# Kernel optimization log

Hardware: AMD Instinct MI355X
Metric: run time of the kernel (lower is better)

The kernel has to match this reference:

```python
import jax, jax.numpy as jnp
import numpy as np

B, N, ND, ED = 4, 24, 13, 12          # batch, num_nodes, node feat dim, edge feat dim
H, NH, HD = 256, 8, 32                # hidden, heads, head dim (H == NH*HD)
L, T = 64, 1000                       # transformer layers, max_timestep
_SCALE = 1.0 / float(np.sqrt(H))      # torch divides by sqrt(node_dim)=sqrt(256)


def _ln(x, g, b):
    m = x.mean(-1, keepdims=True)
    v = ((x - m) ** 2).mean(-1, keepdims=True)
    return (x - m) / jnp.sqrt(v + 1e-5) * g + b


def setup_inputs() -> dict:
    key = jax.random.key(0)
    it = iter(jax.random.split(key, 40))
    def w(*s):
        return (jax.random.normal(next(it), s) * 0.02).astype(jnp.float32)
    z = lambda *s: jnp.zeros(s, jnp.float32)
    o = lambda *s: jnp.ones(s, jnp.float32)
    d = {}
    d['nodes'] = jax.random.normal(next(it), (B, N, ND), jnp.float32)
    d['edges'] = jax.random.normal(next(it), (B, N, N, ED), jnp.float32)
    d['conds'] = jax.random.randint(next(it), (B,), 0, T)
    # input MLPs
    d['inN_w1'] = w(ND, H); d['inN_b1'] = z(H); d['inN_w2'] = w(H, H); d['inN_b2'] = z(H)
    d['inE_w1'] = w(ED, H); d['inE_b1'] = z(H); d['inE_w2'] = w(H, H); d['inE_b2'] = z(H)
    d['inC_w1'] = w(T, H);  d['inC_b1'] = z(H); d['inC_w2'] = w(H, H); d['inC_b2'] = z(H)
    # stacked per-layer params (leading dim L, scanned)
    d['qkv_w'] = w(L, H, 3 * H); d['qkv_b'] = z(L, 3 * H)
    d['no_w'] = w(L, H, H); d['no_b'] = z(L, H)
    d['eo_w'] = w(L, H, H); d['eo_b'] = z(L, H)
    d['ln1n_g'] = o(L, H); d['ln1n_b'] = z(L, H)
    d['ln1e_g'] = o(L, H); d['ln1e_b'] = z(L, H)
    d['mn_w1'] = w(L, H, 4 * H); d['mn_b1'] = z(L, 4 * H)
    d['mn_w2'] = w(L, 4 * H, H); d['mn_b2'] = z(L, H)
    d['me_w1'] = w(L, H, 4 * H); d['me_b1'] = z(L, 4 * H)
    d['me_w2'] = w(L, 4 * H, H); d['me_b2'] = z(L, H)
    d['ln2n_g'] = o(L, H); d['ln2n_b'] = z(L, H)
    d['ln2e_g'] = o(L, H); d['ln2e_b'] = z(L, H)
    # output MLPs
    d['outN_w1'] = w(H, H); d['outN_b1'] = z(H); d['outN_w2'] = w(H, ND); d['outN_b2'] = z(ND)
    d['outE_w1'] = w(H, H); d['outE_b1'] = z(H); d['outE_w2'] = w(H, ED); d['outE_b2'] = z(ED)
    return d


def _forward(nodes, edges, conds,
             inN_w1, inN_b1, inN_w2, inN_b2, inE_w1, inE_b1, inE_w2, inE_b2,
             inC_w1, inC_b1, inC_w2, inC_b2,
             qkv_w, qkv_b, no_w, no_b, eo_w, eo_b,
             ln1n_g, ln1n_b, ln1e_g, ln1e_b,
             mn_w1, mn_b1, mn_w2, mn_b2, me_w1, me_b1, me_w2, me_b2,
             ln2n_g, ln2n_b, ln2e_g, ln2e_b,
             outN_w1, outN_b1, outN_w2, outN_b2, outE_w1, outE_b1, outE_w2, outE_b2):
    relu = jax.nn.relu
    c = jax.nn.one_hot(conds, T, dtype=nodes.dtype)
    c = relu(relu(c @ inC_w1 + inC_b1) @ inC_w2 + inC_b2)          # (B,H)
    n = relu(relu(nodes @ inN_w1 + inN_b1) @ inN_w2 + inN_b2)      # (B,N,H)
    e = relu(relu(edges @ inE_w1 + inE_b1) @ inE_w2 + inE_b2)      # (B,N,N,H)

    def layer(carry, p):
        n, e = carry
        (qw, qb, nw, nb, ew, eb, g1n, b1n, g1e, b1e,
         w1n, bb1n, w2n, bb2n, w1e, bb1e, w2e, bb2e, g2n, b2n, g2e, b2e) = p
        nc = n + c[:, None, :]
        q, k, v = jnp.split(nc @ qw + qb, 3, axis=-1)
        q = q.reshape(B, N, NH, HD); k = k.reshape(B, N, NH, HD); v = v.reshape(B, N, NH, HD)
        s5 = jnp.einsum('bihd,bjhd->bijhd', q, k) * _SCALE          # (B,N,N,NH,HD)
        ne5 = s5 + e.reshape(B, N, N, NH, HD)                       # edge-biased scores
        attn = jax.nn.softmax(ne5.sum(-1), axis=2)                  # (B,N,N,NH)
        wv = jnp.einsum('bijh,bjhd->bihd', attn, v).reshape(B, N, H)
        an = _ln(wv @ nw + nb + n, g1n, b1n)
        ae = _ln(relu(ne5.reshape(B, N, N, H) @ ew + eb) + e, g1e, b1e)
        n2 = _ln(relu(an @ w1n + bb1n) @ w2n + bb2n + an, g2n, b2n)
        e2 = _ln(relu(ae @ w1e + bb1e) @ w2e + bb2e + ae, g2e, b2e)
        return (n2, e2), None

    stacked = (qkv_w, qkv_b, no_w, no_b, eo_w, eo_b, ln1n_g, ln1n_b, ln1e_g, ln1e_b,
               mn_w1, mn_b1, mn_w2, mn_b2, me_w1, me_b1, me_w2, me_b2,
               ln2n_g, ln2n_b, ln2e_g, ln2e_b)
    (n, e), _ = jax.lax.scan(layer, (n, e), stacked)
    out_n = relu(n @ outN_w1 + outN_b1) @ outN_w2 + outN_b2
    out_e = relu(e @ outE_w1 + outE_b1) @ outE_w2 + outE_b2
    return out_n, out_e


def reference(nodes, edges, conds,
              inN_w1, inN_b1, inN_w2, inN_b2, inE_w1, inE_b1, inE_w2, inE_b2,
              inC_w1, inC_b1, inC_w2, inC_b2,
              qkv_w, qkv_b, no_w, no_b, eo_w, eo_b,
              ln1n_g, ln1n_b, ln1e_g, ln1e_b,
              mn_w1, mn_b1, mn_w2, mn_b2, me_w1, me_b1, me_w2, me_b2,
              ln2n_g, ln2n_b, ln2e_g, ln2e_b,
              outN_w1, outN_b1, outN_w2, outN_b2, outE_w1, outE_b1, outE_w2, outE_b2):
    return _forward(nodes, edges, conds,
                    inN_w1, inN_b1, inN_w2, inN_b2, inE_w1, inE_b1, inE_w2, inE_b2,
                    inC_w1, inC_b1, inC_w2, inC_b2,
                    qkv_w, qkv_b, no_w, no_b, eo_w, eo_b,
                    ln1n_g, ln1n_b, ln1e_g, ln1e_b,
                    mn_w1, mn_b1, mn_w2, mn_b2, me_w1, me_b1, me_w2, me_b2,
                    ln2n_g, ln2n_b, ln2e_g, ln2e_b,
                    outN_w1, outN_b1, outN_w2, outN_b2, outE_w1, outE_b1, outE_w2, outE_b2)
```

## Files before the change

kernel.cpp:

```cpp
#include <hip/hip_runtime.h>

typedef _Float16 half_t;
typedef _Float16 f16x8 __attribute__((ext_vector_type(8)));
typedef _Float16 f16x4 __attribute__((ext_vector_type(4)));
typedef float f32x4 __attribute__((ext_vector_type(4)));

#define BB 4
#define NNODE 24
#define NLAYER 64
#define SCALE_QK 0.0625f

#define WS_C     0
#define WS_N     1024
#define WS_QKV   25600
#define WS_E     99328
#define WS_WV    689152
#define WS_NACC  713728
#define WS_AE32  738304
#define WS_AE16  1328128
#define WS_AN16  1623040
#define WS_EPART 1635328
#define EPART_SLICE 589824
#define WS_WTF   3994624
#define SLOT_F16 1376256
#define OFF_QKVT 0
#define OFF_NOT  196608
#define OFF_EOT  262144
#define OFF_MN1T 327680
#define OFF_MN2T 589824
#define OFF_ME1T 851968
#define OFF_ME2T 1114112
#define OFF_INE2T  (3*SLOT_F16)
#define OFF_OUTE1T (3*SLOT_F16 + 65536)

struct Params {
  const float *nodes, *edges; const int* conds;
  const float *inN_w1,*inN_b1,*inN_w2,*inN_b2;
  const float *inE_w1,*inE_b1,*inE_w2,*inE_b2;
  const float *inC_w1,*inC_b1,*inC_w2,*inC_b2;
  const float *qkv_w,*qkv_b,*no_w,*no_b,*eo_w,*eo_b;
  const float *ln1n_g,*ln1n_b,*ln1e_g,*ln1e_b;
  const float *mn_w1,*mn_b1,*mn_w2,*mn_b2,*me_w1,*me_b1,*me_w2,*me_b2;
  const float *ln2n_g,*ln2n_b,*ln2e_g,*ln2e_b;
  const float *outN_w1,*outN_b1,*outN_w2,*outN_b2,*outE_w1,*outE_b1,*outE_w2,*outE_b2;
  float* ws; float* out;
};

template<int NT, int KS, int MT, int LDAH>
__device__ __forceinline__ void gemm_rs_acc(const half_t* __restrict__ WT, int ldb,
                                            const char* __restrict__ A,
                                            f32x4 (&acc)[NT][MT]) {
  const int lane = threadIdx.x & 63;
  const int wv = threadIdx.x >> 6;
  const int l15 = lane & 15;
  const int kg = lane >> 4;
  f16x8 b[NT][KS];
#pragma unroll
  for (int nt = 0; nt < NT; ++nt) {
    const int col = (nt * 8 + wv) * 16 + l15;
#pragma unroll
    for (int ks = 0; ks < KS; ++ks)
      b[nt][ks] = *(const f16x8*)(WT + (size_t)col * ldb + ks * 32 + kg * 8);
  }
#pragma unroll
  for (int m = 0; m < MT; ++m) {
    f16x8 a[KS];
    const int row = m * 16 + l15;
#pragma unroll
    for (int ks = 0; ks < KS; ++ks)
      a[ks] = *(const f16x8*)(A + row * (LDAH * 2) + (((ks * 32 + kg * 8) * 2) ^ ((row & 7) << 4)));
#pragma unroll
    for (int ks = 0; ks < KS; ++ks)
#pragma unroll
      for (int nt = 0; nt < NT; ++nt)
        acc[nt][m] = __builtin_amdgcn_mfma_f32_16x16x32_f16(a[ks], b[nt][ks], acc[nt][m], 0, 0, 0);
  }
}

template<int NT, int KS, int MT, int LDAH, typename EPI>
__device__ __forceinline__ void gemm_rs(const half_t* __restrict__ WT, int ldb,
                                        const char* __restrict__ A, EPI epi) {
  f32x4 acc[NT][MT];
#pragma unroll
  for (int nt = 0; nt < NT; ++nt)
#pragma unroll
    for (int m = 0; m < MT; ++m) {
      f32x4 z = {0.f, 0.f, 0.f, 0.f};
      acc[nt][m] = z;
    }
  gemm_rs_acc<NT, KS, MT, LDAH>(WT, ldb, A, acc);
#pragma unroll
  for (int nt = 0; nt < NT; ++nt)
#pragma unroll
    for (int m = 0; m < MT; ++m)
      epi(nt, m, acc[nt][m]);
}

template<int NTW, int KT, int MT, int LDA, int LDB, typename EPI>
__device__ __forceinline__ void run_gemm_s(const half_t* __restrict__ WT,
                                           const char* __restrict__ A,
                                           EPI epi) {
  const int lane = threadIdx.x & 63;
  const int wv = threadIdx.x >> 6;
  const int l15 = lane & 15;
  const int kg = lane >> 4;
  constexpr int NC = KT / 8;
// ... 19 lines not shown
    f16x8 a[8][MT];
#pragma unroll
    for (int q = 0; q < 8; ++q) {
      const int k0 = (kc * 8 + q) * 32 + kg * 8;
#pragma unroll
      for (int m = 0; m < MT; ++m) {
        const int row = m * 16 + l15;
        a[q][m] = *(const f16x8*)(A + row * (LDA * 2) + ((k0 * 2) ^ ((row & 7) << 4)));
      }
    }
#pragma unroll
    for (int n = 0; n < NTW; ++n) {
      const int c = kc * NTW + n;
      if (c + 1 < TC) ldb(c + 1, (c + 1) & 1);
#pragma unroll
      for (int q = 0; q < 8; ++q)
#pragma unroll
        for (int m = 0; m < MT; ++m)
          acc[n][m] = __builtin_amdgcn_mfma_f32_16x16x32_f16(a[q][m], bb[c & 1][q], acc[n][m], 0, 0, 0);
    }
  }
#pragma unroll
  for (int n = 0; n < NTW; ++n) epi(n, acc[n]);
}

__device__ void conv_matrix_tile(const float* __restrict__ src, half_t* __restrict__ dst,
                                 int K, int Nn, int tk, int tn, char* smem) {
  float* tl = (float*)smem;
  const int t = threadIdx.x;
  const int c = t & 63;
  const int r0 = t >> 6;
  for (int r = r0; r < 64; r += 8)
    tl[r * 65 + c] = src[(size_t)(tk * 64 + r) * Nn + tn * 64 + c];
  __syncthreads();
  for (int r = r0; r < 64; r += 8)
    dst[(size_t)(tn * 64 + r) * K + tk * 64 + c] = (half_t)tl[c * 65 + r];
  __syncthreads();
}

__device__ void conv_layer_tile(const Params& p, half_t* slot, int lw, int tile, char* smem) {
  if (tile < 48)       { conv_matrix_tile(p.qkv_w + (size_t)lw*196608, slot+OFF_QKVT, 256, 768, tile & 3, tile >> 2, smem); }
  else if (tile < 64)  { int t2 = tile-48;  conv_matrix_tile(p.no_w  + (size_t)lw*65536,  slot+OFF_NOT,  256, 256, t2 & 3,  t2 >> 2, smem); }
  else if (tile < 80)  { int t2 = tile-64;  conv_matrix_tile(p.eo_w  + (size_t)lw*65536,  slot+OFF_EOT,  256, 256, t2 & 3,  t2 >> 2, smem); }
  else if (tile < 144) { int t2 = tile-80;  conv_matrix_tile(p.mn_w1 + (size_t)lw*262144, slot+OFF_MN1T, 256, 1024, t2 & 3, t2 >> 2, smem); }
  else if (tile < 208) { int t2 = tile-144; conv_matrix_tile(p.mn_w2 + (size_t)lw*262144, slot+OFF_MN2T, 1024, 256, t2 & 15, t2 >> 4, smem); }
  else if (tile < 272) { int t2 = tile-208; conv_matrix_tile(p.me_w1 + (size_t)lw*262144, slot+OFF_ME1T, 256, 1024, t2 & 3, t2 >> 2, smem); }
  else                 { int t2 = tile-272; conv_matrix_tile(p.me_w2 + (size_t)lw*262144, slot+OFF_ME2T, 1024, 256, t2 & 15, t2 >> 4, smem); }
}

__global__ __launch_bounds__(512, 2) void k_embedA(Params p) {
  __shared__ __align__(16) char smem[17024];
  const int bid = blockIdx.x, tid = threadIdx.x;
  float* ws = p.ws;
  half_t* wt = (half_t*)(ws + WS_WTF);
  if (bid < 4) {
    const int b = bid;
    const int cond = p.conds[b];
    float* t1 = (float*)smem;
    if (tid < 256) t1[tid] = fmaxf(p.inC_w1[(size_t)cond * 256 + tid] + p.inC_b1[tid], 0.f);
    __syncthreads();
    if (tid < 256) {
      float s = p.inC_b2[tid];
      for (int k = 0; k < 256; ++k) s += t1[k] * p.inC_w2[(size_t)k * 256 + tid];
      ws[WS_C + b * 256 + tid] = fmaxf(s, 0.f);
    }
  } else {
    for (int job = bid - 4; job < 704; job += 128) {
      if (job < 336)      conv_layer_tile(p, wt, 0, job, smem);
      else if (job < 672) conv_layer_tile(p, wt + SLOT_F16, 1, job - 336, smem);
      else if (job < 688) { int t2 = job - 672; conv_matrix_tile(p.inE_w2,  wt + OFF_INE2T,  256, 256, t2 & 3, t2 >> 2, smem); }
      else                { int t2 = job - 688; conv_matrix_tile(p.outE_w1, wt + OFF_OUTE1T, 256, 256, t2 & 3, t2 >> 2, smem); }
    }
  }
}

__global__ __launch_bounds__(512, 2) void k_embedB(Params p) {
  __shared__ __align__(16) char smem[24640];
  const int bid = blockIdx.x, tid = threadIdx.x;
  const int lane = tid & 63, wv = tid >> 6, l15 = lane & 15, kg = lane >> 4;
  float* ws = p.ws;
  half_t* wt = (half_t*)(ws + WS_WTF);
  float* e0 = ws + WS_E;
  float* n0 = ws + WS_N;
  float* qkv0 = ws + WS_QKV;
  if (bid < 96) {
    const int b = bid / NNODE, i = bid % NNODE;
    float* eb = (float*)smem;
    char* t16 = smem + 2048;
    for (int idx = tid; idx < 24 * 12; idx += 512)
      eb[idx] = p.edges[((size_t)(b * NNODE + i) * NNODE + idx / 12) * 12 + idx % 12];
    __syncthreads();
    for (int idx = tid; idx < 32 * 32; idx += 512) {
      int r = idx >> 5, kb = idx & 31, k0 = kb * 8;
      f16x8 v;
#pragma unroll
      for (int j = 0; j < 8; ++j) v[j] = (half_t)0.f;
      if (r < NNODE) {
#pragma unroll
        for (int j = 0; j < 8; ++j) {
          int col = k0 + j;
          float s = p.inE_b1[col];
          for (int kk = 0; kk < 12; ++kk) s += eb[r * 12 + kk] * p.inE_w1[kk * 256 + col];
          v[j] = (half_t)fmaxf(s, 0.f);
        }
      }
      *(f16x8*)(t16 + r * 512 + ((k0 * 2) ^ ((r & 7) << 4))) = v;
    }
    __syncthreads();
    run_gemm_s<2, 8, 2, 256, 256>(wt + OFF_INE2T, t16,
      [&](int n, f32x4 (&accn)[2]) {
        const int col = (n * 8 + wv) * 16 + l15;
        const float bcol = p.inE_b2[col];
#pragma unroll
        for (int m = 0; m < 2; ++m)
#pragma unroll
          for (int r4 = 0; r4 < 4; ++r4) {
            const int row = m * 16 + kg * 4 + r4;
            if (row < NNODE)
              e0[((size_t)(b * NNODE + i) * NNODE + row) * 256 + col] = fmaxf(accn[m][r4] + bcol, 0.f);
          }
      });
  } else {
    const int nb = bid - 96, b = nb >> 1, hf = nb & 1, i0 = hf * 12;
    float* nd = (float*)smem;
    float* t1 = (float*)(smem + 1024);
    char* nc16 = smem + 16384;
    for (int idx = tid; idx < 12 * 13; idx += 512)
      nd[(idx / 13) * 16 + (idx % 13)] = p.nodes[(size_t)(b * NNODE + i0 + idx / 13) * 13 + idx % 13];
    __syncthreads();
    for (int idx = tid; idx < 12 * 256; idx += 512) {
      int r = idx >> 8, col = idx & 255;
      float s = p.inN_b1[col];
      for (int kk = 0; kk < 13; ++kk) s += nd[r * 16 + kk] * p.inN_w1[kk * 256 + col];
      t1[r * 257 + col] = fmaxf(s, 0.f);
    }
    __syncthreads();
    {
      int col = tid & 255, rh = tid >> 8;
      float a6[6] = {0.f, 0.f, 0.f, 0.f, 0.f, 0.f};
      for (int k = 0; k < 256; ++k) {
        float w = p.inN_w2[(size_t)k * 256 + col];
#pragma unroll
        for (int r = 0; r < 6; ++r) a6[r] += t1[(rh * 6 + r) * 257 + k] * w;
      }
      const float* cb = ws + WS_C + b * 256;
#pragma unroll
      for (int r = 0; r < 6; ++r) {
        int row = rh * 6 + r;
        float y = fmaxf(a6[r] + p.inN_b2[col], 0.f);
        n0[(size_t)(b * NNODE + i0 + row) * 256 + col] = y;
        *(half_t*)(nc16 + row * 512 + ((col * 2) ^ ((row & 7) << 4))) = (half_t)(y + cb[col]);
      }
      if (rh == 0)
        for (int row = 12; row < 16; ++row)
          *(half_t*)(nc16 + row * 512 + ((col * 2) ^ ((row & 7) << 4))) = (half_t)0.f;
    }
    __syncthreads();
    run_gemm_s<6, 8, 1, 256, 256>(wt + OFF_QKVT, nc16,
      [&](int n, f32x4 (&accn)[1]) {
        const int col = (n * 8 + wv) * 16 + l15;
#pragma unroll
        for (int r4 = 0; r4 < 4; ++r4) {
          const int row = kg * 4 + r4;
          if (row < 12)
            qkv0[(size_t)(b * NNODE + i0 + row) * 768 + col] = accn[0][r4] + p.qkv_b[col];
        }
      });
  }
}

__global__ __launch_bounds__(512, 2) void k_attn(Params p, int lyr) {
  __shared__ __align__(16) char smem[94464];
  const int bid = blockIdx.x, tid = threadIdx.x;
  const int lane = tid & 63, wv = tid >> 6, l15 = lane & 15, kg = lane >> 4;
  float* ws = p.ws;
  half_t* wt = (half_t*)(ws + WS_WTF);
  const float* qkv_in = ws + WS_QKV;
  const half_t* slot = wt + (size_t)(lyr % 3) * SLOT_F16;

  if (bid >= 96) {
    if (lyr + 2 < NLAYER) {
      half_t* dslot = wt + (size_t)((lyr + 2) % 3) * SLOT_F16;
      for (int tile = bid - 96; tile < 336; tile += 126)
        conv_layer_tile(p, dslot, lyr + 2, tile, smem);
    }
    return;
  }
  const int b = bid / NNODE, i = bid % NNODE;
  const size_t rowbase = (size_t)(b * NNODE + i) * NNODE;
  char* ne5 = smem;
  float* e32 = (float*)(smem + 16384);
  float* v32 = (float*)(smem + 41344);
  float* psum = (float*)(smem + 65920);
  float* sc = (float*)(smem + 68992);
  float* aef = (float*)(smem + 69760);
  float* ae32 = ws + WS_AE32;
  half_t* ae16g = (half_t*)(ws + WS_AE16);
  const half_t* epart = (const half_t*)(ws + WS_EPART);

  for (int idx = tid; idx < 32 * 32; idx += 512) {
    int r = idx >> 5, kb = idx & 31, k0 = kb * 8;
    f16x8 v;
#pragma unroll
    for (int j = 0; j < 8; ++j) v[j] = (half_t)0.f;
    if (r < NNODE) {
      const size_t row = rowbase + r;
      float x[8];
      if (lyr == 0) {
        const f32x4 a = *(const f32x4*)(ws + WS_E + row * 256 + k0);
        const f32x4 b4 = *(const f32x4*)(ws + WS_E + row * 256 + k0 + 4);
#pragma unroll
        for (int j = 0; j < 4; ++j) { x[j] = a[j]; x[4 + j] = b4[j]; }
      } else {
        const float* mb2 = p.me_b2 + (size_t)(lyr - 1) * 256;
        const f32x4 a = *(const f32x4*)(ae32 + row * 256 + k0);
        const f32x4 b4 = *(const f32x4*)(ae32 + row * 256 + k0 + 4);
#pragma unroll
        for (int j = 0; j < 4; ++j) { x[j] = a[j] + mb2[k0 + j]; x[4 + j] = b4[j] + mb2[k0 + 4 + j]; }
#pragma unroll
        for (int hb = 0; hb < 8; ++hb) {
          f16x8 pv = *(const f16x8*)(epart + (size_t)hb * EPART_SLICE + row * 256 + k0);
#pragma unroll
          for (int j = 0; j < 8; ++j) x[j] += (float)pv[j];
        }
        float s = 0.f, s2 = 0.f;
#pragma unroll
        for (int j = 0; j < 8; ++j) { s += x[j]; s2 += x[j] * x[j]; }
#pragma unroll
        for (int off = 16; off; off >>= 1) { s += __shfl_xor(s, off); s2 += __shfl_xor(s2, off); }
        float mean = s * (1.f / 256.f);
        float rstd = rsqrtf(s2 * (1.f / 256.f) - mean * mean + 1e-5f);
        const float* g = p.ln2e_g + (size_t)(lyr - 1) * 256;
        const float* bv = p.ln2e_b + (size_t)(lyr - 1) * 256;
#pragma unroll
        for (int j = 0; j < 8; ++j) x[j] = (x[j] - mean) * rstd * g[k0 + j] + bv[k0 + j];
      }
      const float* qp = qkv_in + (size_t)(b * NNODE + i) * 768 + k0;
      const float* kp = qkv_in + (size_t)(b * NNODE + r) * 768 + 256 + k0;
      f32x4 q0 = *(const f32x4*)qp, q1 = *(const f32x4*)(qp + 4);
      f32x4 k0v = *(const f32x4*)kp, k1v = *(const f32x4*)(kp + 4);
      float ps = 0.f;
#pragma unroll
      for (int j = 0; j < 4; ++j) {
        float f0 = SCALE_QK * q0[j] * k0v[j] + x[j];
        float f1 = SCALE_QK * q1[j] * k1v[j] + x[4 + j];
        v[j] = (half_t)f0; v[4 + j] = (half_t)f1;
        ps += f0 + f1;
      }
#pragma unroll
      for (int j = 0; j < 4; ++j) { e32[r * 260 + k0 + j] = x[j]; e32[r * 260 + k0 + 4 + j] = x[4 + j]; }
      psum[r * 32 + kb] = ps;
    }
    *(f16x8*)(ne5 + r * 512 + ((k0 * 2) ^ ((r & 7) << 4))) = v;
  }
  __syncthreads();
  for (int idx = tid; idx < 24 * 256; idx += 512) {
    int j = idx >> 8, d = idx & 255;
    v32[j * 256 + d] = qkv_in[(size_t)(b * NNODE + j) * 768 + 512 + d];
  }
  if (tid < 192) {
    int hq = tid & 7;
    sc[tid] = psum[(tid >> 3) * 32 + hq * 4] + psum[(tid >> 3) * 32 + hq * 4 + 1] +
              psum[(tid >> 3) * 32 + hq * 4 + 2] + psum[(tid >> 3) * 32 + hq * 4 + 3];
  }
  __syncthreads();
  if (tid < 8) {
    const int h = tid;
    float mx = -1e30f;
#pragma unroll
    for (int j = 0; j < 24; ++j) mx = fmaxf(mx, sc[j * 8 + h]);
    float ex[24]; float ssum = 0.f;
#pragma unroll
    for (int j = 0; j < 24; ++j) { ex[j] = __expf(sc[j * 8 + h] - mx); ssum += ex[j]; }
    float inv = 1.f / ssum;
#pragma unroll
    for (int j = 0; j < 24; ++j) sc[j * 8 + h] = ex[j] * inv;
  }
  __syncthreads();
  if (tid < 256) {
    const int d = tid, h = d >> 5;
    float a = 0.f;
#pragma unroll
    for (int j = 0; j < 24; ++j) a += sc[j * 8 + h] * v32[j * 256 + d];
    ws[WS_WV + (size_t)(b * NNODE + i) * 256 + d] = a;
  }
  {
    const float* eob = p.eo_b + (size_t)lyr * 256;
    gemm_rs<2, 8, 2, 256>(slot + OFF_EOT, 256, ne5,
      [&](int nt, int m, f32x4 v) {
        const int col = (nt * 8 + wv) * 16 + l15;
#pragma unroll
        for (int r4 = 0; r4 < 4; ++r4) {
          const int row = m * 16 + kg * 4 + r4;
          if (row < NNODE)
            aef[row * 257 + col] = fmaxf(v[r4] + eob[col], 0.f) + e32[row * 260 + col];
        }
      });
  }
  __syncthreads();
  {
    const float* g = p.ln1e_g + (size_t)lyr * 256;
    const float* bv = p.ln1e_b + (size_t)lyr * 256;
    for (int r = wv; r < NNODE; r += 8) {
      float x[4];
#pragma unroll
      for (int j = 0; j < 4; ++j) x[j] = aef[r * 257 + lane * 4 + j];
      float s = x[0] + x[1] + x[2] + x[3];
      float s2 = x[0]*x[0] + x[1]*x[1] + x[2]*x[2] + x[3]*x[3];
#pragma unroll
      for (int off = 32; off; off >>= 1) { s += __shfl_xor(s, off); s2 += __shfl_xor(s2, off); }
      float mean = s * (1.f / 256.f);
      float rstd = rsqrtf(s2 * (1.f / 256.f) - mean * mean + 1e-5f);
      f16x4 hv; f32x4 yv;
#pragma unroll
      for (int j = 0; j < 4; ++j) {
        int c = lane * 4 + j;
        float y = (x[j] - mean) * rstd * g[c] + bv[c];
        yv[j] = y; hv[j] = (half_t)y;
      }
      *(f32x4*)(ae32 + (rowbase + r) * 256 + lane * 4) = yv;
      *(f16x4*)(ae16g + (rowbase + r) * 256 + lane * 4) = hv;
    }
  }
}

__global__ __launch_bounds__(512, 2) void k_mlp1(Params p, int lyr) {
  __shared__ __align__(16) char smem[73728];
  const int bid = blockIdx.x, tid = threadIdx.x;
  const int lane = tid & 63, wv = tid >> 6, l15 = lane & 15, kg = lane >> 4;
  float* ws = p.ws;
  half_t* wt = (half_t*)(ws + WS_WTF);
  const half_t* slot = wt + (size_t)(lyr % 3) * SLOT_F16;

  if (bid < 192) {
    const int rb = bid >> 3, hb = bid & 7;
    const int row0 = rb * 96;
    char* A16 = smem;
    char* hl = smem + 49152;
    const half_t* aeg = (const half_t*)(ws + WS_AE16) + (size_t)row0 * 256;
    for (int idx = tid; idx < 96 * 32; idx += 512) {
      int r = idx >> 5, c8 = idx & 31;
      f16x8 v = *(const f16x8*)(aeg + r * 256 + c8 * 8);
      *(f16x8*)(A16 + r * 512 + ((c8 * 16) ^ ((r & 7) << 4))) = v;
    }
    __syncthreads();
    const float* mb1 = p.me_b1 + (size_t)lyr * 1024 + hb * 128;
    gemm_rs<1, 8, 6, 256>(slot + OFF_ME1T + (size_t)(hb * 128) * 256, 256, A16,
      [&](int nt, int m, f32x4 v) {
        const int colb = wv * 16 + l15;
        const float bc = mb1[colb];
#pragma unroll
        for (int r4 = 0; r4 < 4; ++r4) {
          const int row = m * 16 + kg * 4 + r4;
          *(half_t*)(hl + row * 256 + ((colb * 2) ^ ((row & 7) << 4))) = (half_t)fmaxf(v[r4] + bc, 0.f);
        }
      });
    __syncthreads();
    half_t* ep = (half_t*)(ws + WS_EPART) + (size_t)hb * EPART_SLICE + (size_t)row0 * 256;
    gemm_rs<2, 4, 6, 128>(slot + OFF_ME2T + hb * 128, 1024, hl,
      [&](int nt, int m, f32x4 v) {
        const int col = (nt * 8 + wv) * 16 + l15;
#pragma unroll
        for (int r4 = 0; r4 < 4; ++r4)
          ep[(size_t)(m * 16 + kg * 4 + r4) * 256 + col] = (half_t)v[r4];
      });
  } else {
    const int nb = bid - 192, r0 = nb * 12;
    char* A16 = smem;
    float* nin = (float*)(smem + 8192);
    float* anf = (float*)(smem + 20528);
    float* n_acc = ws + WS_NACC;
    {
      for (int r = wv; r < 12; r += 8) {
        const int row = r0 + r;
        const int c = lane * 4;
        if (lyr == 0) {
          f32x4 v = *(const f32x4*)(ws + WS_N + (size_t)row * 256 + c);
          *(f32x4*)(nin + r * 257 + c) = v;
        } else {
          f32x4 x = *(const f32x4*)(n_acc + (size_t)row * 256 + c);
          float s = x[0] + x[1] + x[2] + x[3];
          float s2 = x[0]*x[0] + x[1]*x[1] + x[2]*x[2] + x[3]*x[3];
#pragma unroll
          for (int off = 32; off; off >>= 1) { s += __shfl_xor(s, off); s2 += __shfl_xor(s2, off); }
          float mean = s * (1.f / 256.f);
          float rstd = rsqrtf(s2 * (1.f / 256.f) - mean * mean + 1e-5f);
          const float* g = p.ln2n_g + (size_t)(lyr - 1) * 256;
          const float* bv = p.ln2n_b + (size_t)(lyr - 1) * 256;
          f32x4 y;
#pragma unroll
          for (int j = 0; j < 4; ++j) y[j] = (x[j] - mean) * rstd * g[c + j] + bv[c + j];
          *(f32x4*)(nin + r * 257 + c) = y;
        }
      }
    }
    for (int idx = tid; idx < 16 * 32; idx += 512) {
      int r = idx >> 5, c8 = idx & 31;
      f16x8 v;
      if (r < 12) {
        const float* sp = ws + WS_WV + (size_t)(r0 + r) * 256 + c8 * 8;
        f32x4 a = *(const f32x4*)sp, b4 = *(const f32x4*)(sp + 4);
#pragma unroll
        for (int j = 0; j < 4; ++j) { v[j] = (half_t)a[j]; v[4 + j] = (half_t)b4[j]; }
      } else {
#pragma unroll
        for (int j = 0; j < 8; ++j) v[j] = (half_t)0.f;
      }
      *(f16x8*)(A16 + r * 512 + ((c8 * 16) ^ ((r & 7) << 4))) = v;
    }
    __syncthreads();
    {
      const float* nob = p.no_b + (size_t)lyr * 256;
      gemm_rs<2, 8, 1, 256>(slot + OFF_NOT, 256, A16,
        [&](int nt, int m, f32x4 v) {
          const int col = (nt * 8 + wv) * 16 + l15;
#pragma unroll
          for (int r4 = 0; r4 < 4; ++r4) {
            const int row = kg * 4 + r4;
            if (row < 12)
              anf[row * 257 + col] = v[r4] + nob[col] + nin[row * 257 + col];
          }
        });
    }
    __syncthreads();
    {
      const float* g = p.ln1n_g + (size_t)lyr * 256;
      const float* bv = p.ln1n_b + (size_t)lyr * 256;
      const float* mb2 = p.mn_b2 + (size_t)lyr * 256;
      half_t* an16g = (half_t*)(ws + WS_AN16);
      for (int r = wv; r < 12; r += 8) {
        float x[4];
#pragma unroll
        for (int j = 0; j < 4; ++j) x[j] = anf[r * 257 + lane * 4 + j];
        float s = x[0] + x[1] + x[2] + x[3];
        float s2 = x[0]*x[0] + x[1]*x[1] + x[2]*x[2] + x[3]*x[3];
#pragma unroll
        for (int off = 32; off; off >>= 1) { s += __shfl_xor(s, off); s2 += __shfl_xor(s2, off); }
        float mean = s * (1.f / 256.f);
        float rstd = rsqrtf(s2 * (1.f / 256.f) - mean * mean + 1e-5f);
        f16x4 hv; f32x4 av;
#pragma unroll
        for (int j = 0; j < 4; ++j) {
          int c = lane * 4 + j;
          float y = (x[j] - mean) * rstd * g[c] + bv[c];
          hv[j] = (half_t)y;
          av[j] = y + mb2[c];
        }
        *(f16x4*)(an16g + (size_t)(r0 + r) * 256 + lane * 4) = hv;
        *(f32x4*)(ws + WS_NACC + (size_t)(r0 + r) * 256 + lane * 4) = av;
      }
    }
  }
}

__global__ __launch_bounds__(512, 2) void k_mn(Params p, int lyr) {
  __shared__ __align__(16) char smem[73728];
  const int hb = blockIdx.x, tid = threadIdx.x;
  const int lane = tid & 63, wv = tid >> 6, l15 = lane & 15, kg = lane >> 4;
  float* ws = p.ws;
  half_t* wt = (half_t*)(ws + WS_WTF);
  const half_t* slot = wt + (size_t)(lyr % 3) * SLOT_F16;
  char* A16 = smem;
  char* hl = smem + 49152;
  const half_t* ang = (const half_t*)(ws + WS_AN16);
  for (int idx = tid; idx < 96 * 32; idx += 512) {
    int r = idx >> 5, c8 = idx & 31;
    f16x8 v = *(const f16x8*)(ang + (size_t)r * 256 + c8 * 8);
    *(f16x8*)(A16 + r * 512 + ((c8 * 16) ^ ((r & 7) << 4))) = v;
  }
  __syncthreads();
  const float* mb1 = p.mn_b1 + (size_t)lyr * 1024 + hb * 128;
  gemm_rs<1, 8, 6, 256>(slot + OFF_MN1T + (size_t)(hb * 128) * 256, 256, A16,
    [&](int nt, int m, f32x4 v) {
      const int colb = wv * 16 + l15;
      const float bc = mb1[colb];
#pragma unroll
      for (int r4 = 0; r4 < 4; ++r4) {
        const int row = m * 16 + kg * 4 + r4;
        *(half_t*)(hl + row * 256 + ((colb * 2) ^ ((row & 7) << 4))) = (half_t)fmaxf(v[r4] + bc, 0.f);
      }
    });
  __syncthreads();
  float* n_acc = ws + WS_NACC;
  gemm_rs<2, 4, 6, 128>(slot + OFF_MN2T + hb * 128, 1024, hl,
    [&](int nt, int m, f32x4 v) {
      const int col = (nt * 8 + wv) * 16 + l15;
#pragma unroll
      for (int r4 = 0; r4 < 4; ++r4)
        atomicAdd(&n_acc[(size_t)(m * 16 + kg * 4 + r4) * 256 + col], v[r4]);
    });
}

__global__ __launch_bounds__(512, 2) void k_qkv(Params p, int lyr) {
  __shared__ __align__(16) char smem[49152];
  const int bid = blockIdx.x, tid = threadIdx.x;
  const int lane = tid & 63, wv = tid >> 6, l15 = lane & 15, kg = lane >> 4;
  float* ws = p.ws;
  half_t* wt = (half_t*)(ws + WS_WTF);
  char* nc16 = smem;
  const float* n_acc = ws + WS_NACC;
  const float* g = p.ln2n_g + (size_t)lyr * 256;
  const float* bv = p.ln2n_b + (size_t)lyr * 256;
  for (int r = wv; r < 96; r += 8) {
    const int c = lane * 4;
    const float* cb = ws + WS_C + (r / NNODE) * 256;
    f32x4 x = *(const f32x4*)(n_acc + (size_t)r * 256 + c);
    float s = x[0] + x[1] + x[2] + x[3];
    float s2 = x[0]*x[0] + x[1]*x[1] + x[2]*x[2] + x[3]*x[3];
#pragma unroll
    for (int off = 32; off; off >>= 1) { s += __shfl_xor(s, off); s2 += __shfl_xor(s2, off); }
    float mean = s * (1.f / 256.f);
    float rstd = rsqrtf(s2 * (1.f / 256.f) - mean * mean + 1e-5f);
    f16x4 hv;
#pragma unroll
    for (int j = 0; j < 4; ++j)
      hv[j] = (half_t)((x[j] - mean) * rstd * g[c + j] + bv[c + j] + cb[c + j]);
    *(f16x4*)(nc16 + r * 512 + ((c * 2) ^ ((r & 7) << 4))) = hv;
  }
  __syncthreads();
  const int col0 = bid * 128;
  const half_t* slotN = wt + (size_t)((lyr + 1) % 3) * SLOT_F16;
  const float* qb = p.qkv_b + (size_t)(lyr + 1) * 768;
  float* qkv_out = ws + WS_QKV;
  gemm_rs<1, 8, 6, 256>(slotN + OFF_QKVT + (size_t)col0 * 256, 256, nc16,
    [&](int nt, int m, f32x4 v) {
      const int col = col0 + wv * 16 + l15;
#pragma unroll
      for (int r4 = 0; r4 < 4; ++r4) {
        const int row = m * 16 + kg * 4 + r4;
        qkv_out[(size_t)row * 768 + col] = v[r4] + qb[col];
      }
    });
}

__global__ __launch_bounds__(512, 2) void k_out(Params p) {
  __shared__ __align__(16) char smem[49472];
  const int bid = blockIdx.x, tid = threadIdx.x;
  const int lane = tid & 63, wv = tid >> 6, l15 = lane & 15, kg = lane >> 4;
  float* ws = p.ws;
  half_t* wt = (half_t*)(ws + WS_WTF);
  const float* ae32 = ws + WS_AE32;
  const half_t* epart = (const half_t*)(ws + WS_EPART);
  if (bid < 96) {
    const int b = bid / NNODE, i = bid % NNODE;
    const size_t rowbase = (size_t)(b * NNODE + i) * NNODE;
    char* A16 = smem;
    float* h2f = (float*)(smem + 16384);
    const float* mb2 = p.me_b2 + (size_t)63 * 256;
    const float* g = p.ln2e_g + (size_t)63 * 256;
    const float* bvv = p.ln2e_b + (size_t)63 * 256;
    for (int idx = tid; idx < 32 * 32; idx += 512) {
      int r = idx >> 5, kb = idx & 31, k0 = kb * 8;
      f16x8 v;
#pragma unroll
      for (int j = 0; j < 8; ++j) v[j] = (half_t)0.f;
      if (r < NNODE) {
        const size_t row = rowbase + r;
        float x[8];
        const f32x4 a = *(const f32x4*)(ae32 + row * 256 + k0);
        const f32x4 b4 = *(const f32x4*)(ae32 + row * 256 + k0 + 4);
#pragma unroll
        for (int j = 0; j < 4; ++j) { x[j] = a[j] + mb2[k0 + j]; x[4 + j] = b4[j] + mb2[k0 + 4 + j]; }
#pragma unroll
        for (int hb = 0; hb < 8; ++hb) {
          f16x8 pv = *(const f16x8*)(epart + (size_t)hb * EPART_SLICE + row * 256 + k0);
#pragma unroll
          for (int j = 0; j < 8; ++j) x[j] += (float)pv[j];
        }
        float s = 0.f, s2 = 0.f;
#pragma unroll
        for (int j = 0; j < 8; ++j) { s += x[j]; s2 += x[j] * x[j]; }
#pragma unroll
        for (int off = 16; off; off >>= 1) { s += __shfl_xor(s, off); s2 += __shfl_xor(s2, off); }
        float mean = s * (1.f / 256.f);
        float rstd = rsqrtf(s2 * (1.f / 256.f) - mean * mean + 1e-5f);
#pragma unroll
        for (int j = 0; j < 8; ++j)
          v[j] = (half_t)((x[j] - mean) * rstd * g[k0 + j] + bvv[k0 + j]);
      }
      *(f16x8*)(A16 + r * 512 + ((k0 * 2) ^ ((r & 7) << 4))) = v;
    }
    __syncthreads();
    run_gemm_s<2, 8, 2, 256, 256>(wt + OFF_OUTE1T, A16,
      [&](int n, f32x4 (&accn)[2]) {
        const int col = (n * 8 + wv) * 16 + l15;
#pragma unroll
        for (int m = 0; m < 2; ++m)
#pragma unroll
          for (int r4 = 0; r4 < 4; ++r4) {
            const int row = m * 16 + kg * 4 + r4;
            h2f[row * 257 + col] = (row < NNODE) ? fmaxf(accn[m][r4] + p.outE_b1[col], 0.f) : 0.f;
          }
      });
    __syncthreads();
    for (int pr = tid; pr < 24 * 12; pr += 512) {
      int j = pr / 12, oc = pr % 12;
      float s = p.outE_b2[oc];
      for (int k = 0; k < 256; ++k) s += h2f[j * 257 + k] * p.outE_w2[k * 12 + oc];
      p.out[1248 + ((size_t)(b * NNODE + i) * NNODE + j) * 12 + oc] = s;
    }
  } else {
    const int nb = bid - 96, bq = nb >> 1, hf = nb & 1, i0 = hf * 12;
    float* nl = (float*)smem;
    float* t1f = (float*)(smem + 12544);
    const float* n_acc = ws + WS_NACC;
    const float* g = p.ln2n_g + (size_t)63 * 256;
    const float* bvv = p.ln2n_b + (size_t)63 * 256;
    for (int r = wv; r < 12; r += 8) {
      const int row = bq * NNODE + i0 + r;
      const int c = lane * 4;
      f32x4 x = *(const f32x4*)(n_acc + (size_t)row * 256 + c);
      float s = x[0] + x[1] + x[2] + x[3];
      float s2 = x[0]*x[0] + x[1]*x[1] + x[2]*x[2] + x[3]*x[3];
#pragma unroll
      for (int off = 32; off; off >>= 1) { s += __shfl_xor(s, off); s2 += __shfl_xor(s2, off); }
      float mean = s * (1.f / 256.f);
      float rstd = rsqrtf(s2 * (1.f / 256.f) - mean * mean + 1e-5f);
      f32x4 y;
#pragma unroll
      for (int j = 0; j < 4; ++j) y[j] = (x[j] - mean) * rstd * g[c + j] + bvv[c + j];
      *(f32x4*)(nl + r * 257 + c) = y;
    }
    __syncthreads();
    {
      int col = tid & 255, rh = tid >> 8;
      float a6[6] = {0.f, 0.f, 0.f, 0.f, 0.f, 0.f};
      for (int k = 0; k < 256; ++k) {
        float w = p.outN_w1[(size_t)k * 256 + col];
#pragma unroll
        for (int r = 0; r < 6; ++r) a6[r] += nl[(rh * 6 + r) * 257 + k] * w;
      }
#pragma unroll
      for (int r = 0; r < 6; ++r)
        t1f[(rh * 6 + r) * 257 + col] = fmaxf(a6[r] + p.outN_b1[col], 0.f);
    }
    __syncthreads();
    for (int pr = tid; pr < 12 * 13; pr += 512) {
      int il = pr / 13, oc = pr % 13;
      float s = p.outN_b2[oc];
      for (int k = 0; k < 256; ++k) s += t1f[il * 257 + k] * p.outN_w2[k * 13 + oc];
      p.out[((size_t)(bq * NNODE) + i0 + il) * 13 + oc] = s;
    }
  }
}

extern "C" void kernel_launch(void* const* d_in, const int* in_sizes, int n_in,
                              void* d_out, int out_size, void* d_ws, size_t ws_size,
                              hipStream_t stream) {
  (void)in_sizes; (void)n_in; (void)out_size; (void)ws_size;
  Params p;
  const float* const* fi = (const float* const*)d_in;
  p.nodes = fi[0]; p.edges = fi[1]; p.conds = (const int*)d_in[2];
  p.inN_w1 = fi[3]; p.inN_b1 = fi[4]; p.inN_w2 = fi[5]; p.inN_b2 = fi[6];
  p.inE_w1 = fi[7]; p.inE_b1 = fi[8]; p.inE_w2 = fi[9]; p.inE_b2 = fi[10];
  p.inC_w1 = fi[11]; p.inC_b1 = fi[12]; p.inC_w2 = fi[13]; p.inC_b2 = fi[14];
  p.qkv_w = fi[15]; p.qkv_b = fi[16]; p.no_w = fi[17]; p.no_b = fi[18];
  p.eo_w = fi[19]; p.eo_b = fi[20];
  p.ln1n_g = fi[21]; p.ln1n_b = fi[22]; p.ln1e_g = fi[23]; p.ln1e_b = fi[24];
  p.mn_w1 = fi[25]; p.mn_b1 = fi[26]; p.mn_w2 = fi[27]; p.mn_b2 = fi[28];
  p.me_w1 = fi[29]; p.me_b1 = fi[30]; p.me_w2 = fi[31]; p.me_b2 = fi[32];
  p.ln2n_g = fi[33]; p.ln2n_b = fi[34]; p.ln2e_g = fi[35]; p.ln2e_b = fi[36];
  p.outN_w1 = fi[37]; p.outN_b1 = fi[38]; p.outN_w2 = fi[39]; p.outN_b2 = fi[40];
  p.outE_w1 = fi[41]; p.outE_b1 = fi[42]; p.outE_w2 = fi[43]; p.outE_b2 = fi[44];
  p.ws = (float*)d_ws; p.out = (float*)d_out;

  k_embedA<<<dim3(132), dim3(512), 0, stream>>>(p);
  k_embedB<<<dim3(104), dim3(512), 0, stream>>>(p);
  for (int l = 0; l < NLAYER; ++l) {
    k_attn<<<dim3(222), dim3(512), 0, stream>>>(p, l);
    k_mlp1<<<dim3(200), dim3(512), 0, stream>>>(p, l);
    k_mn<<<dim3(8), dim3(512), 0, stream>>>(p, l);
    if (l + 1 < NLAYER)
      k_qkv<<<dim3(6), dim3(512), 0, stream>>>(p, l);
  }
  k_out<<<dim3(104), dim3(512), 0, stream>>>(p);
}
```

Baseline: 3.602 ms.

## Fuse QKV projection and node-output LN into attention kernel, cut launches per layer

Each attention block now recomputes the full QKV projection for its batch (24 rows) in shared memory as fp16, and also performs the node-output projection plus LN1 for its own row. This removes the separate k_qkv kernel and the node-output part of k_mlp1, and the node MLP moves into the merged k_mlp kernel, leaving two launches per layer instead of four. Node accumulators are double-buffered so the next layer can read them while the current one writes. The trade-off is redundant QKV GEMM work (24x per batch), larger shared memory per block that may lower occupancy, and fp16 rounding of q/k/v.

Measured after the change: 2.953 ms (median of 2 runs). 18.0% less time.

```diff
diff --git a/kernel.cpp b/kernel.cpp
--- a/kernel.cpp
+++ b/kernel.cpp
@@ -12,16 +12,15 @@
 
 #define WS_C     0
 #define WS_N     1024
-#define WS_QKV   25600
-#define WS_E     99328
-#define WS_WV    689152
-#define WS_NACC  713728
-#define WS_AE32  738304
-#define WS_AE16  1328128
-#define WS_AN16  1623040
-#define WS_EPART 1635328
+#define WS_NACC  25600
+#define NACC_STRIDE 24576
+#define WS_E     74752
+#define WS_AE32  664576
+#define WS_AE16  1254400
+#define WS_AN16  1549312
+#define WS_EPART 1561600
 #define EPART_SLICE 589824
-#define WS_WTF   3994624
+#define WS_WTF   3920896
 #define SLOT_F16 1376256
 #define OFF_QKVT 0
 #define OFF_NOT  196608
@@ -207,7 +206,6 @@
   half_t* wt = (half_t*)(ws + WS_WTF);
   float* e0 = ws + WS_E;
   float* n0 = ws + WS_N;
-  float* qkv0 = ws + WS_QKV;
   if (bid < 96) {
     const int b = bid / NNODE, i = bid % NNODE;
     float* eb = (float*)smem;
@@ -249,7 +247,6 @@
     const int nb = bid - 96, b = nb >> 1, hf = nb & 1, i0 = hf * 12;
     float* nd = (float*)smem;
     float* t1 = (float*)(smem + 1024);
-    char* nc16 = smem + 16384;
     for (int idx = tid; idx < 12 * 13; idx += 512)
       nd[(idx / 13) * 16 + (idx % 13)] = p.nodes[(size_t)(b * NNODE + i0 + idx / 13) * 13 + idx % 13];
     __syncthreads();
@@ -268,39 +265,21 @@
 #pragma unroll
         for (int r = 0; r < 6; ++r) a6[r] += t1[(rh * 6 + r) * 257 + k] * w;
       }
-      const float* cb = ws + WS_C + b * 256;
 #pragma unroll
       for (int r = 0; r < 6; ++r) {
         int row = rh * 6 + r;
-        float y = fmaxf(a6[r] + p.inN_b2[col], 0.f);
-        n0[(size_t)(b * NNODE + i0 + row) * 256 + col] = y;
-        *(half_t*)(nc16 + row * 512 + ((col * 2) ^ ((row & 7) << 4))) = (half_t)(y + cb[col]);
-      }
-      if (rh == 0)
-        for (int row = 12; row < 16; ++row)
-          *(half_t*)(nc16 + row * 512 + ((col * 2) ^ ((row & 7) << 4))) = (half_t)0.f;
-    }
-    __syncthreads();
-    run_gemm_s<6, 8, 1, 256, 256>(wt + OFF_QKVT, nc16,
-      [&](int n, f32x4 (&accn)[1]) {
-        const int col = (n * 8 + wv) * 16 + l15;
-#pragma unroll
-        for (int r4 = 0; r4 < 4; ++r4) {
-          const int row = kg * 4 + r4;
-          if (row < 12)
-            qkv0[(size_t)(b * NNODE + i0 + row) * 768 + col] = accn[0][r4] + p.qkv_b[col];
-        }
-      });
+        n0[(size_t)(b * NNODE + i0 + row) * 256 + col] = fmaxf(a6[r] + p.inN_b2[col], 0.f);
+      }
+    }
   }
 }
 
 __global__ __launch_bounds__(512, 2) void k_attn(Params p, int lyr) {
-  __shared__ __align__(16) char smem[94464];
+  __shared__ __align__(16) char smem[139488];
   const int bid = blockIdx.x, tid = threadIdx.x;
   const int lane = tid & 63, wv = tid >> 6, l15 = lane & 15, kg = lane >> 4;
   float* ws = p.ws;
   half_t* wt = (half_t*)(ws + WS_WTF);
-  const float* qkv_in = ws + WS_QKV;
   const half_t* slot = wt + (size_t)(lyr % 3) * SLOT_F16;
 
   if (bid >= 96) {
@@ -313,16 +292,70 @@
   }
   const int b = bid / NNODE, i = bid % NNODE;
   const size_t rowbase = (size_t)(b * NNODE + i) * NNODE;
-  char* ne5 = smem;
-  float* e32 = (float*)(smem + 16384);
-  float* v32 = (float*)(smem + 41344);
-  float* psum = (float*)(smem + 65920);
-  float* sc = (float*)(smem + 68992);
-  float* aef = (float*)(smem + 69760);
+  char* nc16 = smem;
+  half_t* qkv16 = (half_t*)(smem + 16384);
+  char* ne5 = smem + 65536;
+  float* e32 = (float*)(smem + 81920);
+  float* psum = (float*)(smem + 106880);
+  float* sc = (float*)(smem + 109952);
+  float* wvl = (float*)(smem + 110720);
+  float* ni = (float*)(smem + 111744);
+  float* anr = (float*)(smem + 112768);
+  float* aef = (float*)(smem + 114816);
   float* ae32 = ws + WS_AE32;
   half_t* ae16g = (half_t*)(ws + WS_AE16);
   const half_t* epart = (const half_t*)(ws + WS_EPART);
-
+  const float* nacc_in = ws + WS_NACC + ((lyr + 1) & 1) * NACC_STRIDE;
+  float* nacc_out = ws + WS_NACC + (lyr & 1) * NACC_STRIDE;
+  const float* cb = ws + WS_C + b * 256;
+
+  for (int r = wv; r < 32; r += 8) {
+    const int c = lane * 4;
+    f16x4 hv;
+    if (r < NNODE) {
+      f32x4 y;
+      if (lyr == 0) {
+        y = *(const f32x4*)(ws + WS_N + (size_t)(b * NNODE + r) * 256 + c);
+      } else {
+        f32x4 x = *(const f32x4*)(nacc_in + (size_t)(b * NNODE + r) * 256 + c);
+        float s = x[0] + x[1] + x[2] + x[3];
+        float s2 = x[0]*x[0] + x[1]*x[1] + x[2]*x[2] + x[3]*x[3];
+#pragma unroll
+        for (int off = 32; off; off >>= 1) { s += __shfl_xor(s, off); s2 += __shfl_xor(s2, off); }
+        float mean = s * (1.f / 256.f);
+        float rstd = rsqrtf(s2 * (1.f / 256.f) - mean * mean + 1e-5f);
+        const float* g = p.ln2n_g + (size_t)(lyr - 1) * 256;
+        const float* bv = p.ln2n_b + (size_t)(lyr - 1) * 256;
+#pragma unroll
+        for (int j = 0; j < 4; ++j) y[j] = (x[j] - mean) * rstd * g[c + j] + bv[c + j];
+      }
+      if (r == i) *(f32x4*)(ni + c) = y;
+#pragma unroll
+      for (int j = 0; j < 4; ++j) hv[j] = (half_t)(y[j] + cb[c + j]);
+    } else {
+#pragma unroll
+      for (int j = 0; j < 4; ++j) hv[j] = (half_t)0.f;
+    }
+    *(f16x4*)(nc16 + r * 512 + ((lane * 8) ^ ((r & 7) << 4))) = hv;
+  }
+  __syncthreads();
+  {
+    const float* qb = p.qkv_b + (size_t)lyr * 768;
+#pragma unroll
+    for (int nn = 0; nn < 3; ++nn) {
+      gemm_rs<2, 8, 2, 256>(slot + OFF_QKVT + (size_t)(nn * 256) * 256, 256, nc16,
+        [&](int nt, int m, f32x4 v) {
+          const int gcol = nn * 256 + (nt * 8 + wv) * 16 + l15;
+          const float bc = qb[gcol];
+#pragma unroll
+          for (int r4 = 0; r4 < 4; ++r4) {
+            const int row = m * 16 + kg * 4 + r4;
+            qkv16[(size_t)row * 768 + gcol] = (half_t)(v[r4] + bc);
+          }
+        });
+    }
+  }
+  __syncthreads();
   for (int idx = tid; idx < 32 * 32; idx += 512) {
     int r = idx >> 5, kb = idx & 31, k0 = kb * 8;
     f16x8 v;
@@ -360,29 +393,21 @@
 #pragma unroll
         for (int j = 0; j < 8; ++j) x[j] = (x[j] - mean) * rstd * g[k0 + j] + bv[k0 + j];
       }
-      const float* qp = qkv_in + (size_t)(b * NNODE + i) * 768 + k0;
-      const float* kp = qkv_in + (size_t)(b * NNODE + r) * 768 + 256 + k0;
-      f32x4 q0 = *(const f32x4*)qp, q1 = *(const f32x4*)(qp + 4);
-      f32x4 k0v = *(const f32x4*)kp, k1v = *(const f32x4*)(kp + 4);
+      f16x8 q8 = *(const f16x8*)(qkv16 + (size_t)i * 768 + k0);
+      f16x8 k8 = *(const f16x8*)(qkv16 + (size_t)r * 768 + 256 + k0);
       float ps = 0.f;
 #pragma unroll
-      for (int j = 0; j < 4; ++j) {
-        float f0 = SCALE_QK * q0[j] * k0v[j] + x[j];
-        float f1 = SCALE_QK * q1[j] * k1v[j] + x[4 + j];
-        v[j] = (half_t)f0; v[4 + j] = (half_t)f1;
-        ps += f0 + f1;
-      }
-#pragma unroll
-      for (int j = 0; j < 4; ++j) { e32[r * 260 + k0 + j] = x[j]; e32[r * 260 + k0 + 4 + j] = x[4 + j]; }
+      for (int j = 0; j < 8; ++j) {
+        float f = SCALE_QK * (float)q8[j] * (float)k8[j] + x[j];
+        v[j] = (half_t)f;
+        ps += f;
+        e32[r * 260 + k0 + j] = x[j];
+      }
       psum[r * 32 + kb] = ps;
     }
     *(f16x8*)(ne5 + r * 512 + ((k0 * 2) ^ ((r & 7) << 4))) = v;
   }
   __syncthreads();
-  for (int idx = tid; idx < 24 * 256; idx += 512) {
-    int j = idx >> 8, d = idx & 255;
-    v32[j * 256 + d] = qkv_in[(size_t)(b * NNODE + j) * 768 + 512 + d];
-  }
   if (tid < 192) {
     int hq = tid & 7;
     sc[tid] = psum[(tid >> 3) * 32 + hq * 4] + psum[(tid >> 3) * 32 + hq * 4 + 1] +
@@ -406,8 +431,8 @@
     const int d = tid, h = d >> 5;
     float a = 0.f;
 #pragma unroll
-    for (int j = 0; j < 24; ++j) a += sc[j * 8 + h] * v32[j * 256 + d];
-    ws[WS_WV + (size_t)(b * NNODE + i) * 256 + d] = a;
+    for (int j = 0; j < 24; ++j) a += sc[j * 8 + h] * (float)qkv16[(size_t)j * 768 + 512 + d];
+    wvl[d] = a;
   }
   {
     const float* eob = p.eo_b + (size_t)lyr * 256;
@@ -447,9 +472,51 @@
       *(f16x4*)(ae16g + (rowbase + r) * 256 + lane * 4) = hv;
     }
   }
-}
-
-__global__ __launch_bounds__(512, 2) void k_mlp1(Params p, int lyr) {
+  {
+    const half_t* NOT_ = slot + OFF_NOT;
+    int c = tid & 255, hf = tid >> 8;
+    float s = 0.f;
+    const half_t* wp = NOT_ + (size_t)c * 256 + hf * 128;
+#pragma unroll
+    for (int k8 = 0; k8 < 16; ++k8) {
+      f16x8 w8 = *(const f16x8*)(wp + k8 * 8);
+#pragma unroll
+      for (int j = 0; j < 8; ++j) s += wvl[hf * 128 + k8 * 8 + j] * (float)w8[j];
+    }
+    anr[hf * 256 + c] = s;
+  }
+  __syncthreads();
+  if (wv == 0) {
+    const float* nob = p.no_b + (size_t)lyr * 256;
+    const float* g = p.ln1n_g + (size_t)lyr * 256;
+    const float* bv = p.ln1n_b + (size_t)lyr * 256;
+    const float* mb2 = p.mn_b2 + (size_t)lyr * 256;
+    float x[4];
+#pragma unroll
+    for (int j = 0; j < 4; ++j) {
+      int c = lane * 4 + j;
+      x[j] = anr[c] + anr[256 + c] + nob[c] + ni[c];
+    }
+    float s = x[0] + x[1] + x[2] + x[3];
+    float s2 = x[0]*x[0] + x[1]*x[1] + x[2]*x[2] + x[3]*x[3];
+#pragma unroll
+    for (int off = 32; off; off >>= 1) { s += __shfl_xor(s, off); s2 += __shfl_xor(s2, off); }
+    float mean = s * (1.f / 256.f);
+    float rstd = rsqrtf(s2 * (1.f / 256.f) - mean * mean + 1e-5f);
+    f16x4 hv; f32x4 av;
+#pragma unroll
+    for (int j = 0; j < 4; ++j) {
+      int c = lane * 4 + j;
+      float y = (x[j] - mean) * rstd * g[c] + bv[c];
+      hv[j] = (half_t)y;
+      av[j] = y + mb2[c];
+    }
+    *(f16x4*)((half_t*)(ws + WS_AN16) + (size_t)(b * NNODE + i) * 256 + lane * 4) = hv;
+    *(f32x4*)(nacc_out + (size_t)(b * NNODE + i) * 256 + lane * 4) = av;
+  }
+}
+
+__global__ __launch_bounds__(512, 2) void k_mlp(Params p, int lyr) {
   __shared__ __align__(16) char smem[73728];
   const int bid = blockIdx.x, tid = threadIdx.x;
   const int lane = tid & 63, wv = tid >> 6, l15 = lane & 15, kg = lane >> 4;
@@ -490,172 +557,37 @@
           ep[(size_t)(m * 16 + kg * 4 + r4) * 256 + col] = (half_t)v[r4];
       });
   } else {
-    const int nb = bid - 192, r0 = nb * 12;
+    const int hb = bid - 192;
     char* A16 = smem;
-    float* nin = (float*)(smem + 8192);
-    float* anf = (float*)(smem + 20528);
-    float* n_acc = ws + WS_NACC;
-    {
-      for (int r = wv; r < 12; r += 8) {
-        const int row = r0 + r;
-        const int c = lane * 4;
-        if (lyr == 0) {
-          f32x4 v = *(const f32x4*)(ws + WS_N + (size_t)row * 256 + c);
-          *(f32x4*)(nin + r * 257 + c) = v;
-        } else {
-          f32x4 x = *(const f32x4*)(n_acc + (size_t)row * 256 + c);
-          float s = x[0] + x[1] + x[2] + x[3];
-          float s2 = x[0]*x[0] + x[1]*x[1] + x[2]*x[2] + x[3]*x[3];
-#pragma unroll
-          for (int off = 32; off; off >>= 1) { s += __shfl_xor(s, off); s2 += __shfl_xor(s2, off); }
-          float mean = s * (1.f / 256.f);
-          float rstd = rsqrtf(s2 * (1.f / 256.f) - mean * mean + 1e-5f);
-          const float* g = p.ln2n_g + (size_t)(lyr - 1) * 256;
-          const float* bv = p.ln2n_b + (size_t)(lyr - 1) * 256;
-          f32x4 y;
-#pragma unroll
-          for (int j = 0; j < 4; ++j) y[j] = (x[j] - mean) * rstd * g[c + j] + bv[c + j];
-          *(f32x4*)(nin + r * 257 + c) = y;
+    char* hl = smem + 49152;
+    const half_t* ang = (const half_t*)(ws + WS_AN16);
+    for (int idx = tid; idx < 96 * 32; idx += 512) {
+      int r = idx >> 5, c8 = idx & 31;
+      f16x8 v = *(const f16x8*)(ang + (size_t)r * 256 + c8 * 8);
+      *(f16x8*)(A16 + r * 512 + ((c8 * 16) ^ ((r & 7) << 4))) = v;
+    }
+    __syncthreads();
+    const float* mb1 = p.mn_b1 + (size_t)lyr * 1024 + hb * 128;
+    gemm_rs<1, 8, 6, 256>(slot + OFF_MN1T + (size_t)(hb * 128) * 256, 256, A16,
+      [&](int nt, int m, f32x4 v) {
+        const int colb = wv * 16 + l15;
+        const float bc = mb1[colb];
+#pragma unroll
+        for (int r4 = 0; r4 < 4; ++r4) {
+          const int row = m * 16 + kg * 4 + r4;
+          *(half_t*)(hl + row * 256 + ((colb * 2) ^ ((row & 7) << 4))) = (half_t)fmaxf(v[r4] + bc, 0.f);
         }
-      }
-    }
-    for (int idx = tid; idx < 16 * 32; idx += 512) {
-      int r = idx >> 5, c8 = idx & 31;
-      f16x8 v;
-      if (r < 12) {
-        const float* sp = ws + WS_WV + (size_t)(r0 + r) * 256 + c8 * 8;
-        f32x4 a = *(const f32x4*)sp, b4 = *(const f32x4*)(sp + 4);
-#pragma unroll
-        for (int j = 0; j < 4; ++j) { v[j] = (half_t)a[j]; v[4 + j] = (half_t)b4[j]; }
-      } else {
-#pragma unroll
-        for (int j = 0; j < 8; ++j) v[j] = (half_t)0.f;
-      }
-      *(f16x8*)(A16 + r * 512 + ((c8 * 16) ^ ((r & 7) << 4))) = v;
-    }
-    __syncthreads();
-    {
-      const float* nob = p.no_b + (size_t)lyr * 256;
-      gemm_rs<2, 8, 1, 256>(slot + OFF_NOT, 256, A16,
-        [&](int nt, int m, f32x4 v) {
-          const int col = (nt * 8 + wv) * 16 + l15;
-#pragma unroll
-          for (int r4 = 0; r4 < 4; ++r4) {
-            const int row = kg * 4 + r4;
-            if (row < 12)
-              anf[row * 257 + col] = v[r4] + nob[col] + nin[row * 257 + col];
-          }
-        });
-    }
-    __syncthreads();
-    {
-      const float* g = p.ln1n_g + (size_t)lyr * 256;
-      const float* bv = p.ln1n_b + (size_t)lyr * 256;
-      const float* mb2 = p.mn_b2 + (size_t)lyr * 256;
-      half_t* an16g = (half_t*)(ws + WS_AN16);
-      for (int r = wv; r < 12; r += 8) {
-        float x[4];
-#pragma unroll
-        for (int j = 0; j < 4; ++j) x[j] = anf[r * 257 + lane * 4 + j];
-        float s = x[0] + x[1] + x[2] + x[3];
-        float s2 = x[0]*x[0] + x[1]*x[1] + x[2]*x[2] + x[3]*x[3];
-#pragma unroll
-        for (int off = 32; off; off >>= 1) { s += __shfl_xor(s, off); s2 += __shfl_xor(s2, off); }
-        float mean = s * (1.f / 256.f);
-        float rstd = rsqrtf(s2 * (1.f / 256.f) - mean * mean + 1e-5f);
-        f16x4 hv; f32x4 av;
-#pragma unroll
-        for (int j = 0; j < 4; ++j) {
-          int c = lane * 4 + j;
-          float y = (x[j] - mean) * rstd * g[c] + bv[c];
-          hv[j] = (half_t)y;
-          av[j] = y + mb2[c];
-        }
-        *(f16x4*)(an16g + (size_t)(r0 + r) * 256 + lane * 4) = hv;
-        *(f32x4*)(ws + WS_NACC + (size_t)(r0 + r) * 256 + lane * 4) = av;
-      }
-    }
-  }
-}
-
-__global__ __launch_bounds__(512, 2) void k_mn(Params p, int lyr) {
-  __shared__ __align__(16) char smem[73728];
-  const int hb = blockIdx.x, tid = threadIdx.x;
-  const int lane = tid & 63, wv = tid >> 6, l15 = lane & 15, kg = lane >> 4;
-  float* ws = p.ws;
-  half_t* wt = (half_t*)(ws + WS_WTF);
-  const half_t* slot = wt + (size_t)(lyr % 3) * SLOT_F16;
-  char* A16 = smem;
-  char* hl = smem + 49152;
-  const half_t* ang = (const half_t*)(ws + WS_AN16);
-  for (int idx = tid; idx < 96 * 32; idx += 512) {
-    int r = idx >> 5, c8 = idx & 31;
-    f16x8 v = *(const f16x8*)(ang + (size_t)r * 256 + c8 * 8);
-    *(f16x8*)(A16 + r * 512 + ((c8 * 16) ^ ((r & 7) << 4))) = v;
-  }
-  __syncthreads();
-  const float* mb1 = p.mn_b1 + (size_t)lyr * 1024 + hb * 128;
-  gemm_rs<1, 8, 6, 256>(slot + OFF_MN1T + (size_t)(hb * 128) * 256, 256, A16,
-    [&](int nt, int m, f32x4 v) {
-      const int colb = wv * 16 + l15;
-      const float bc = mb1[colb];
-#pragma unroll
-      for (int r4 = 0; r4 < 4; ++r4) {
-        const int row = m * 16 + kg * 4 + r4;
-        *(half_t*)(hl + row * 256 + ((colb * 2) ^ ((row & 7) << 4))) = (half_t)fmaxf(v[r4] + bc, 0.f);
-      }
-    });
-  __syncthreads();
-  float* n_acc = ws + WS_NACC;
-  gemm_rs<2, 4, 6, 128>(slot + OFF_MN2T + hb * 128, 1024, hl,
-    [&](int nt, int m, f32x4 v) {
-      const int col = (nt * 8 + wv) * 16 + l15;
-#pragma unroll
-      for (int r4 = 0; r4 < 4; ++r4)
-        atomicAdd(&n_acc[(size_t)(m * 16 + kg * 4 + r4) * 256 + col], v[r4]);
-    });
-}
-
-__global__ __launch_bounds__(512, 2) void k_qkv(Params p, int lyr) {
-  __shared__ __align__(16) char smem[49152];
-  const int bid = blockIdx.x, tid = threadIdx.x;
-  const int lane = tid & 63, wv = tid >> 6, l15 = lane & 15, kg = lane >> 4;
-  float* ws = p.ws;
-  half_t* wt = (half_t*)(ws + WS_WTF);
-  char* nc16 = smem;
-  const float* n_acc = ws + WS_NACC;
-  const float* g = p.ln2n_g + (size_t)lyr * 256;
-  const float* bv = p.ln2n_b + (size_t)lyr * 256;
-  for (int r = wv; r < 96; r += 8) {
-    const int c = lane * 4;
-    const float* cb = ws + WS_C + (r / NNODE) * 256;
-    f32x4 x = *(const f32x4*)(n_acc + (size_t)r * 256 + c);
-    float s = x[0] + x[1] + x[2] + x[3];
-    float s2 = x[0]*x[0] + x[1]*x[1] + x[2]*x[2] + x[3]*x[3];
-#pragma unroll
-    for (int off = 32; off; off >>= 1) { s += __shfl_xor(s, off); s2 += __shfl_xor(s2, off); }
-    float mean = s * (1.f / 256.f);
-    float rstd = rsqrtf(s2 * (1.f / 256.f) - mean * mean + 1e-5f);
-    f16x4 hv;
-#pragma unroll
-    for (int j = 0; j < 4; ++j)
-      hv[j] = (half_t)((x[j] - mean) * rstd * g[c + j] + bv[c + j] + cb[c + j]);
-    *(f16x4*)(nc16 + r * 512 + ((c * 2) ^ ((r & 7) << 4))) = hv;
-  }
-  __syncthreads();
-  const int col0 = bid * 128;
-  const half_t* slotN = wt + (size_t)((lyr + 1) % 3) * SLOT_F16;
-  const float* qb = p.qkv_b + (size_t)(lyr + 1) * 768;
-  float* qkv_out = ws + WS_QKV;
-  gemm_rs<1, 8, 6, 256>(slotN + OFF_QKVT + (size_t)col0 * 256, 256, nc16,
-    [&](int nt, int m, f32x4 v) {
-      const int col = col0 + wv * 16 + l15;
-#pragma unroll
-      for (int r4 = 0; r4 < 4; ++r4) {
-        const int row = m * 16 + kg * 4 + r4;
-        qkv_out[(size_t)row * 768 + col] = v[r4] + qb[col];
-      }
-    });
+      });
+    __syncthreads();
+    float* nacc_out = ws + WS_NACC + (lyr & 1) * NACC_STRIDE;
+    gemm_rs<2, 4, 6, 128>(slot + OFF_MN2T + hb * 128, 1024, hl,
+      [&](int nt, int m, f32x4 v) {
+        const int col = (nt * 8 + wv) * 16 + l15;
+#pragma unroll
+        for (int r4 = 0; r4 < 4; ++r4)
+          atomicAdd(&nacc_out[(size_t)(m * 16 + kg * 4 + r4) * 256 + col], v[r4]);
+      });
+  }
 }
 
 __global__ __launch_bounds__(512, 2) void k_out(Params p) {
@@ -728,7 +660,7 @@
     const int nb = bid - 96, bq = nb >> 1, hf = nb & 1, i0 = hf * 12;
     float* nl = (float*)smem;
     float* t1f = (float*)(smem + 12544);
-    const float* n_acc = ws + WS_NACC;
+    const float* n_acc = ws + WS_NACC + 1 * NACC_STRIDE;
     const float* g = p.ln2n_g + (size_t)63 * 256;
     const float* bvv = p.ln2n_b + (size_t)63 * 256;
     for (int r = wv; r < 12; r += 8) {
@@ -793,10 +725,7 @@
   k_embedB<<<dim3(104), dim3(512), 0, stream>>>(p);
   for (int l = 0; l < NLAYER; ++l) {
     k_attn<<<dim3(222), dim3(512), 0, stream>>>(p, l);
-    k_mlp1<<<dim3(200), dim3(512), 0, stream>>>(p, l);
-    k_mn<<<dim3(8), dim3(512), 0, stream>>>(p, l);
-    if (l + 1 < NLAYER)
-      k_qkv<<<dim3(6), dim3(512), 0, stream>>>(p, l);
+    k_mlp<<<dim3(200), dim3(512), 0, stream>>>(p, l);
   }
   k_out<<<dim3(104), dim3(512), 0, stream>>>(p);
 }
```
